# Kernel optimization log

Measured on AMD Instinct MI355X. Metric: run time of the kernel, lower is better.

## Reference

```python
import jax, jax.numpy as jnp
import numpy as np


def setup_inputs() -> dict:
    key = jax.random.key(0)
    k1, k2, k3 = jax.random.split(key, 3)
    x = jax.random.normal(k1, (8, 256, 256, 256), dtype=jnp.float32)
    # Conv2d(2, 1, kernel_size=7): kaiming-uniform-like small init
    fan_in = 2 * 7 * 7
    bound = 1.0 / np.sqrt(fan_in)
    conv_w = jax.random.uniform(k2, (1, 2, 7, 7), dtype=jnp.float32, minval=-bound, maxval=bound)
    conv_b = jax.random.uniform(k3, (1,), dtype=jnp.float32, minval=-bound, maxval=bound)
    return {"x": x, "conv_w": conv_w, "conv_b": conv_b}


def reference(x, conv_w, conv_b):
    # channel-wise mean and max -> [B, 2, H, W]
    avg_out = jnp.mean(x, axis=1, keepdims=True)
    max_out = jnp.max(x, axis=1, keepdims=True)
    stacked = jnp.concatenate([avg_out, max_out], axis=1)
    # 7x7 conv, 2->1 channels, padding=3 (SAME)
    attn = jax.lax.conv_general_dilated(
        stacked, conv_w,
        window_strides=(1, 1), padding=((3, 3), (3, 3)),
        dimension_numbers=("NCHW", "OIHW", "NCHW"),
    ) + conv_b[None, :, None, None]
    return jax.nn.sigmoid(attn) * x
```

## Files before the change

### kernel.cpp

```cpp
#include <hip/hip_runtime.h>
#include <math.h>

#define BB 8
#define CC 256
#define HH 256
#define WW 256
#define HWC (HH * WW)
#define G4  (HWC / 4)

#define GB 2

typedef float nf4 __attribute__((ext_vector_type(4)));

__global__ __launch_bounds__(256) void k_stats(const float* __restrict__ x,
                                               float* __restrict__ avgp,
                                               float* __restrict__ maxp,
                                               int bbase) {
    __shared__ float4 ssum[4][64];
    __shared__ float4 smax[4][64];

    const int gi = threadIdx.x & 63;
    const int sp = threadIdx.x >> 6;
    const int G  = blockIdx.x * 64 + gi;
    const int bl = G >> 14;
    const int p4 = G & (G4 - 1);
    const int b  = bbase + bl;

    const float4* x4 = (const float4*)x + (((size_t)b * CC + sp * 64) << 14) + p4;

    float4 v = x4[0];
    float4 s = v, m = v;
#pragma unroll 4
    for (int c = 1; c < 64; ++c) {
        float4 t = x4[(size_t)c << 14];
        s.x += t.x; s.y += t.y; s.z += t.z; s.w += t.w;
        m.x = fmaxf(m.x, t.x); m.y = fmaxf(m.y, t.y);
        m.z = fmaxf(m.z, t.z); m.w = fmaxf(m.w, t.w);
    }
    ssum[sp][gi] = s;
    smax[sp][gi] = m;
    __syncthreads();

    if (threadIdx.x < 64) {
        float4 s0 = ssum[0][threadIdx.x], s1 = ssum[1][threadIdx.x];
        float4 s2 = ssum[2][threadIdx.x], s3 = ssum[3][threadIdx.x];
        float4 m0 = smax[0][threadIdx.x], m1 = smax[1][threadIdx.x];
        float4 m2 = smax[2][threadIdx.x], m3 = smax[3][threadIdx.x];
        const float inv = 1.0f / (float)CC;
        float4 a = { (s0.x + s1.x + s2.x + s3.x) * inv,
                     (s0.y + s1.y + s2.y + s3.y) * inv,
                     (s0.z + s1.z + s2.z + s3.z) * inv,
                     (s0.w + s1.w + s2.w + s3.w) * inv };
        float4 mm = { fmaxf(fmaxf(m0.x, m1.x), fmaxf(m2.x, m3.x)),
                      fmaxf(fmaxf(m0.y, m1.y), fmaxf(m2.y, m3.y)),
                      fmaxf(fmaxf(m0.z, m1.z), fmaxf(m2.z, m3.z)),
                      fmaxf(fmaxf(m0.w, m1.w), fmaxf(m2.w, m3.w)) };
        size_t o = ((size_t)b << 14) + p4 - gi + threadIdx.x;
        ((float4*)avgp)[o] = a;
        ((float4*)maxp)[o] = mm;
    }
}

__global__ __launch_bounds__(256) void k_conv(const float* __restrict__ avgp,
                                              const float* __restrict__ maxp,
                                              const float* __restrict__ cw,
                                              const float* __restrict__ cb,
                                              float* __restrict__ attnp,
                                              int bbase) {
    int t = blockIdx.x * 256 + threadIdx.x + (bbase << 16);
    int b   = t >> 16;
    int pix = t & (HWC - 1);
    int h   = pix >> 8;
    int w   = pix & (WW - 1);

    const float* ap = avgp + ((size_t)b << 16);
    const float* mp = maxp + ((size_t)b << 16);

    float sum = cb[0];
#pragma unroll
    for (int kh = 0; kh < 7; ++kh) {
        int hh = h + kh - 3;
        if ((unsigned)hh >= (unsigned)HH) continue;
#pragma unroll
        for (int kw = 0; kw < 7; ++kw) {
            int ww = w + kw - 3;
            if ((unsigned)ww >= (unsigned)WW) continue;
            int o = (hh << 8) + ww;
            sum = fmaf(cw[kh * 7 + kw],      ap[o], sum);
            sum = fmaf(cw[49 + kh * 7 + kw], mp[o], sum);
        }
    }
    attnp[t] = 1.0f / (1.0f + __expf(-sum));
}

__global__ __launch_bounds__(256) void k_mul(const float* __restrict__ x,
                                             const float* __restrict__ attnp,
                                             float* __restrict__ out,
                                             int bbase) {
    size_t g = ((size_t)blockIdx.x * 256 + threadIdx.x)
             + (((size_t)bbase << 24) >> 2);
    size_t e = g << 2;
    size_t b   = e >> 24;
    size_t pix = e & (size_t)(HWC - 1);

    float4 a = *((const float4*)attnp + (((b << 16) + pix) >> 2));
    float4 v = ((const float4*)x)[g];
    nf4 o = { v.x * a.x, v.y * a.y, v.z * a.z, v.w * a.w };
    __builtin_nontemporal_store(o, (nf4*)out + g);
}

extern "C" void kernel_launch(void* const* d_in, const int* in_sizes, int n_in,
                              void* d_out, int out_size, void* d_ws, size_t ws_size,
                              hipStream_t stream) {
    const float* x  = (const float*)d_in[0];
    const float* cw = (const float*)d_in[1];
    const float* cb = (const float*)d_in[2];
    float* out = (float*)d_out;

    float* avgp  = (float*)d_ws;
    float* maxp  = avgp + (size_t)BB * HWC;
    float* attnp = maxp + (size_t)BB * HWC;

    for (int bbase = 0; bbase < BB; bbase += GB) {
        k_stats<<<GB * G4 / 64, 256, 0, stream>>>(x, avgp, maxp, bbase);
        k_conv<<<GB * HWC / 256, 256, 0, stream>>>(avgp, maxp, cw, cb, attnp, bbase);
        k_mul<<<GB * CC * (HWC / 4) / 256, 256, 0, stream>>>(x, attnp, out, bbase);
    }
}
```

Measured before the change: 311.8 us.

## Drop batch-group launches; use nontemporal loads and 8-channel-per-thread multiply

Replaces the per-two-batch loop of three kernel launches with one launch of each kernel over all eight batches. Stats loads of x become nontemporal, and the multiply kernel now has each thread handle eight channels for one pixel group, loading the attention vector once. This cuts launch overhead and the repeated attention loads. The cost is the cache reuse the grouped schedule was likely built for: with the full 512MB input per pass, the second read of x in the multiply kernel probably comes from HBM instead of the last-level cache, and the nontemporal loads may also discourage caching.

```diff
diff --git a/kernel.cpp b/kernel.cpp
--- a/kernel.cpp
+++ b/kernel.cpp
@@ -8,32 +8,28 @@
 #define HWC (HH * WW)
 #define G4  (HWC / 4)
 
-#define GB 2
-
 typedef float nf4 __attribute__((ext_vector_type(4)));
 
 __global__ __launch_bounds__(256) void k_stats(const float* __restrict__ x,
                                                float* __restrict__ avgp,
-                                               float* __restrict__ maxp,
-                                               int bbase) {
-    __shared__ float4 ssum[4][64];
-    __shared__ float4 smax[4][64];
+                                               float* __restrict__ maxp) {
+    __shared__ nf4 ssum[4][64];
+    __shared__ nf4 smax[4][64];
 
     const int gi = threadIdx.x & 63;
     const int sp = threadIdx.x >> 6;
     const int G  = blockIdx.x * 64 + gi;
-    const int bl = G >> 14;
+    const int b  = G >> 14;
     const int p4 = G & (G4 - 1);
-    const int b  = bbase + bl;
 
-    const float4* x4 = (const float4*)x + (((size_t)b * CC + sp * 64) << 14) + p4;
+    const nf4* x4 = (const nf4*)x + (((size_t)(b * CC + sp * 64)) << 14) + p4;
 
-    float4 v = x4[0];
-    float4 s = v, m = v;
-#pragma unroll 4
+    nf4 v = __builtin_nontemporal_load(x4);
+    nf4 s = v, m = v;
+#pragma unroll 8
     for (int c = 1; c < 64; ++c) {
-        float4 t = x4[(size_t)c << 14];
-        s.x += t.x; s.y += t.y; s.z += t.z; s.w += t.w;
+        nf4 t = __builtin_nontemporal_load(x4 + ((size_t)c << 14));
+        s += t;
         m.x = fmaxf(m.x, t.x); m.y = fmaxf(m.y, t.y);
         m.z = fmaxf(m.z, t.z); m.w = fmaxf(m.w, t.w);
     }
@@ -42,22 +38,21 @@
     __syncthreads();
 
     if (threadIdx.x < 64) {
-        float4 s0 = ssum[0][threadIdx.x], s1 = ssum[1][threadIdx.x];
-        float4 s2 = ssum[2][threadIdx.x], s3 = ssum[3][threadIdx.x];
-        float4 m0 = smax[0][threadIdx.x], m1 = smax[1][threadIdx.x];
-        float4 m2 = smax[2][threadIdx.x], m3 = smax[3][threadIdx.x];
+        nf4 s0 = ssum[0][threadIdx.x], s1 = ssum[1][threadIdx.x];
+        nf4 s2 = ssum[2][threadIdx.x], s3 = ssum[3][threadIdx.x];
+        nf4 m0 = smax[0][threadIdx.x], m1 = smax[1][threadIdx.x];
+        nf4 m2 = smax[2][threadIdx.x], m3 = smax[3][threadIdx.x];
+        nf4 sa = (s0 + s1) + (s2 + s3);
         const float inv = 1.0f / (float)CC;
-        float4 a = { (s0.x + s1.x + s2.x + s3.x) * inv,
-                     (s0.y + s1.y + s2.y + s3.y) * inv,
-                     (s0.z + s1.z + s2.z + s3.z) * inv,
-                     (s0.w + s1.w + s2.w + s3.w) * inv };
-        float4 mm = { fmaxf(fmaxf(m0.x, m1.x), fmaxf(m2.x, m3.x)),
-                      fmaxf(fmaxf(m0.y, m1.y), fmaxf(m2.y, m3.y)),
-                      fmaxf(fmaxf(m0.z, m1.z), fmaxf(m2.z, m3.z)),
-                      fmaxf(fmaxf(m0.w, m1.w), fmaxf(m2.w, m3.w)) };
-        size_t o = ((size_t)b << 14) + p4 - gi + threadIdx.x;
-        ((float4*)avgp)[o] = a;
-        ((float4*)maxp)[o] = mm;
+        nf4 a = sa * inv;
+        nf4 mm;
+        mm.x = fmaxf(fmaxf(m0.x, m1.x), fmaxf(m2.x, m3.x));
+        mm.y = fmaxf(fmaxf(m0.y, m1.y), fmaxf(m2.y, m3.y));
+        mm.z = fmaxf(fmaxf(m0.z, m1.z), fmaxf(m2.z, m3.z));
+        mm.w = fmaxf(fmaxf(m0.w, m1.w), fmaxf(m2.w, m3.w));
+        int group = blockIdx.x * 64 + threadIdx.x;
+        ((nf4*)avgp)[group] = a;
+        ((nf4*)maxp)[group] = mm;
     }
 }
 
@@ -65,9 +60,8 @@
                                               const float* __restrict__ maxp,
                                               const float* __restrict__ cw,
                                               const float* __restrict__ cb,
-                                              float* __restrict__ attnp,
-                                              int bbase) {
-    int t = blockIdx.x * 256 + threadIdx.x + (bbase << 16);
+                                              float* __restrict__ attnp) {
+    int t = blockIdx.x * 256 + threadIdx.x;
     int b   = t >> 16;
     int pix = t & (HWC - 1);
     int h   = pix >> 8;
@@ -95,18 +89,36 @@
 
 __global__ __launch_bounds__(256) void k_mul(const float* __restrict__ x,
                                              const float* __restrict__ attnp,
-                                             float* __restrict__ out,
-                                             int bbase) {
-    size_t g = ((size_t)blockIdx.x * 256 + threadIdx.x)
-             + (((size_t)bbase << 24) >> 2);
-    size_t e = g << 2;
-    size_t b   = e >> 24;
-    size_t pix = e & (size_t)(HWC - 1);
+                                             float* __restrict__ out) {
+    size_t t = (size_t)blockIdx.x * 256 + threadIdx.x;
+    int p4 = (int)(t & (G4 - 1));
+    int r  = (int)(t >> 14);
+    int c8 = r & 31;
+    int b  = r >> 5;
 
-    float4 a = *((const float4*)attnp + (((b << 16) + pix) >> 2));
-    float4 v = ((const float4*)x)[g];
-    nf4 o = { v.x * a.x, v.y * a.y, v.z * a.z, v.w * a.w };
-    __builtin_nontemporal_store(o, (nf4*)out + g);
+    const nf4* x4 = (const nf4*)x;
+    nf4*       o4 = (nf4*)out;
+    size_t base = (((size_t)(b * CC + c8 * 8)) << 14) + p4;
+
+    nf4 a = ((const nf4*)attnp)[((size_t)b << 14) + p4];
+
+    nf4 v0 = __builtin_nontemporal_load(x4 + base + ((size_t)0 << 14));
+    nf4 v1 = __builtin_nontemporal_load(x4 + base + ((size_t)1 << 14));
+    nf4 v2 = __builtin_nontemporal_load(x4 + base + ((size_t)2 << 14));
+    nf4 v3 = __builtin_nontemporal_load(x4 + base + ((size_t)3 << 14));
+    nf4 v4 = __builtin_nontemporal_load(x4 + base + ((size_t)4 << 14));
+    nf4 v5 = __builtin_nontemporal_load(x4 + base + ((size_t)5 << 14));
+    nf4 v6 = __builtin_nontemporal_load(x4 + base + ((size_t)6 << 14));
+    nf4 v7 = __builtin_nontemporal_load(x4 + base + ((size_t)7 << 14));
+
+    __builtin_nontemporal_store(v0 * a, o4 + base + ((size_t)0 << 14));
+    __builtin_nontemporal_store(v1 * a, o4 + base + ((size_t)1 << 14));
+    __builtin_nontemporal_store(v2 * a, o4 + base + ((size_t)2 << 14));
+    __builtin_nontemporal_store(v3 * a, o4 + base + ((size_t)3 << 14));
+    __builtin_nontemporal_store(v4 * a, o4 + base + ((size_t)4 << 14));
+    __builtin_nontemporal_store(v5 * a, o4 + base + ((size_t)5 << 14));
+    __builtin_nontemporal_store(v6 * a, o4 + base + ((size_t)6 << 14));
+    __builtin_nontemporal_store(v7 * a, o4 + base + ((size_t)7 << 14));
 }
 
 extern "C" void kernel_launch(void* const* d_in, const int* in_sizes, int n_in,
@@ -121,9 +133,7 @@
     float* maxp  = avgp + (size_t)BB * HWC;
     float* attnp = maxp + (size_t)BB * HWC;
 
-    for (int bbase = 0; bbase < BB; bbase += GB) {
-        k_stats<<<GB * G4 / 64, 256, 0, stream>>>(x, avgp, maxp, bbase);
-        k_conv<<<GB * HWC / 256, 256, 0, stream>>>(avgp, maxp, cw, cb, attnp, bbase);
-        k_mul<<<GB * CC * (HWC / 4) / 256, 256, 0, stream>>>(x, attnp, out, bbase);
-    }
+    k_stats<<<BB * G4 / 64, 256, 0, stream>>>(x, avgp, maxp);
+    k_conv<<<BB * HWC / 256, 256, 0, stream>>>(avgp, maxp, cw, cb, attnp);
+    k_mul<<<BB * (CC / 8) * G4 / 256, 256, 0, stream>>>(x, attnp, out);
 }
```

After: 285.6 us. 8.4% less time.
